# Kernel tuning notes

Hardware: AMD Instinct MI355X
Metric: run time of the kernel (lower is better)

Reference implementation:

```python
import jax, jax.numpy as jnp
import numpy as np

B, C, OC, H, W = 2, 64, 128, 96, 96
HD, DI, N, R, K = C // 2, C, 16, 2, 4  # VSSBlock: hidden=C/2, d_inner=2*hidden=C, d_state, dt_rank, 4 scan dirs
EPS = 1e-5


def _conv(x, w, b, pad, groups=1):
    y = jax.lax.conv_general_dilated(x, w, (1, 1), pad, feature_group_count=groups,
                                     dimension_numbers=('NCHW', 'OIHW', 'NCHW'))
    return y + b[None, :, None, None]


def _ln(x, w, b):
    m = x.mean(-1, keepdims=True)
    v = x.var(-1, keepdims=True)
    return (x - m) * jax.lax.rsqrt(v + EPS) * w + b


def _selective_scan(xs, dts, Bs, Cs, A, D):
    # xs, dts: (B,K,DI,L); Bs, Cs: (B,K,N,L); A: (K,DI,N); D: (K,DI)
    dts = jax.nn.softplus(dts)

    def step(h, inp):
        u_t, dt_t, B_t, C_t = inp
        dA = jnp.exp(dt_t[..., None] * A)                         # (B,K,DI,N)
        h = dA * h + (dt_t * u_t)[..., None] * B_t[:, :, None, :]
        return h, jnp.einsum('bkdn,bkn->bkd', h, C_t)

    seq = (jnp.moveaxis(xs, -1, 0), jnp.moveaxis(dts, -1, 0),
           jnp.moveaxis(Bs, -1, 0), jnp.moveaxis(Cs, -1, 0))
    h0 = jnp.zeros(xs.shape[:3] + (A.shape[-1],), xs.dtype)
    _, ys = jax.lax.scan(step, h0, seq)
    return jnp.moveaxis(ys, 0, -1) + D[None, :, :, None] * xs


def _vss_block(x, ln_w, ln_b, in_w, conv_w, conv_b, xproj_w, dtproj_w, dtproj_b,
               A_logs, Ds, on_w, on_b, out_w):
    # x: (B,H,W,HD); VMamba SS2D with 4-direction cross-scan + residual
    b, hh, ww, _ = x.shape
    L = hh * ww
    h = _ln(x, ln_w, ln_b)
    xz = h @ in_w                                   # (B,H,W,2*DI)
    xp, z = jnp.split(xz, 2, axis=-1)
    xc = jnp.transpose(xp, (0, 3, 1, 2))            # (B,DI,H,W)
    xc = jax.nn.silu(_conv(xc, conv_w, conv_b, ((1, 1), (1, 1)), groups=DI))
    x_flat = xc.reshape(b, DI, L)
    x_wh = jnp.transpose(xc, (0, 1, 3, 2)).reshape(b, DI, L)
    x2 = jnp.stack([x_flat, x_wh], axis=1)
    xs = jnp.concatenate([x2, jnp.flip(x2, -1)], axis=1)      # (B,4,DI,L)
    x_dbl = jnp.einsum('bkdl,kcd->bkcl', xs, xproj_w)
    dts, Bs, Cs = jnp.split(x_dbl, [R, R + N], axis=2)
    dts = jnp.einsum('bkrl,kdr->bkdl', dts, dtproj_w) + dtproj_b[None, :, :, None]
    A = -jnp.exp(A_logs)
    ys = _selective_scan(xs, dts, Bs, Cs, A, Ds)              # (B,4,DI,L)
    inv = jnp.flip(ys[:, 2:4], -1)
    unwh = lambda t: jnp.transpose(t.reshape(b, DI, ww, hh), (0, 1, 3, 2)).reshape(b, DI, L)
    y = ys[:, 0] + inv[:, 0] + unwh(ys[:, 1]) + unwh(inv[:, 1])
    y = jnp.transpose(y.reshape(b, DI, hh, ww), (0, 2, 3, 1))
    y = _ln(y, on_w, on_b) * jax.nn.silu(z)
    return x + y @ out_w


def _forward(x, ms_dw33_w, ms_dw33_b, ms_in_w, ms_in_b, ms_scale,
             vss_ln_w, vss_ln_b, vss_in_w, vss_conv_w, vss_conv_b, vss_xproj_w,
             vss_dtproj_w, vss_dtproj_b, vss_A_logs, vss_Ds, vss_on_w, vss_on_b, vss_out_w,
             ma_conv_w, ma_conv_b, adw_h_w, adw_h_b, adw_w_w, adw_w_b,
             pw_w, pw_b, bn_w, bn_b, bn_mean, bn_var):
    vss = (vss_ln_w, vss_ln_b, vss_in_w, vss_conv_w, vss_conv_b, vss_xproj_w,
           vss_dtproj_w, vss_dtproj_b, vss_A_logs, vss_Ds, vss_on_w, vss_on_b, vss_out_w)
    # --- MambaSplit (shared VSSBlock applied to both channel halves) ---
    xd = _conv(x, ms_dw33_w, ms_dw33_b, ((1, 1), (1, 1)), groups=C)
    x1, x2 = jnp.split(xd, 2, axis=1)

    def branch(xp):
        y = _vss_block(jnp.transpose(xp, (0, 2, 3, 1)), *vss)
        return ms_scale * xp + jnp.transpose(y, (0, 3, 1, 2))

    xm = jnp.concatenate([branch(x1), branch(x2)], axis=1)
    m = xm.mean((2, 3), keepdims=True)
    v = xm.var((2, 3), keepdims=True)
    xm = (xm - m) * jax.lax.rsqrt(v + EPS) * ms_in_w[None, :, None, None] + ms_in_b[None, :, None, None]
    xm = jax.nn.leaky_relu(xm, 0.01)
    # --- MaxAvg (global avg+max pool -> 3x3 conv on 1x1 map -> sigmoid gate) ---
    pooled = jnp.concatenate([x.mean((2, 3), keepdims=True), x.max((2, 3), keepdims=True)], axis=1)
    gate = jax.nn.sigmoid(_conv(pooled, ma_conv_w, ma_conv_b, ((1, 1), (1, 1))))
    xs_ = xm + gate * x
    # --- AxialDW ---
    xs_ = xs_ + _conv(xs_, adw_h_w, adw_h_b, ((1, 1), (0, 0)), groups=C) \
              + _conv(xs_, adw_w_w, adw_w_b, ((0, 0), (1, 1)), groups=C)
    # --- BN (eval) + ReLU, 1x1 conv, 2x2 maxpool ---
    skip = jax.nn.relu((xs_ - bn_mean[None, :, None, None]) * jax.lax.rsqrt(bn_var[None, :, None, None] + EPS)
                       * bn_w[None, :, None, None] + bn_b[None, :, None, None])
    out = _conv(skip, pw_w, pw_b, ((0, 0), (0, 0)))
    down = jax.lax.reduce_window(out, -jnp.inf, jax.lax.max, (1, 1, 2, 2), (1, 1, 2, 2), 'VALID')
    return down, skip


def setup_inputs() -> dict:
    key = jax.random.key(0)
    ks = jax.random.split(key, 16)
    r = lambda i, shape, s=0.02: jax.random.normal(ks[i], shape, jnp.float32) * s
    return {
        'x': jax.random.normal(ks[0], (B, C, H, W), jnp.float32),
        'ms_dw33_w': r(1, (C, 1, 3, 3), 0.1), 'ms_dw33_b': jnp.zeros(C),
        'ms_in_w': jnp.ones(C), 'ms_in_b': jnp.zeros(C),
        'ms_scale': jnp.ones((1,)),
        'vss_ln_w': jnp.ones(HD), 'vss_ln_b': jnp.zeros(HD),
        'vss_in_w': r(2, (HD, 2 * DI)),
        'vss_conv_w': r(3, (DI, 1, 3, 3), 0.1), 'vss_conv_b': jnp.zeros(DI),
        'vss_xproj_w': r(4, (K, R + 2 * N, DI)),
        'vss_dtproj_w': r(5, (K, DI, R), 0.1), 'vss_dtproj_b': r(6, (K, DI), 0.1),
        'vss_A_logs': jnp.tile(jnp.log(jnp.arange(1, N + 1, dtype=jnp.float32)), (K, DI, 1)),
        'vss_Ds': jnp.ones((K, DI)),
        'vss_on_w': jnp.ones(DI), 'vss_on_b': jnp.zeros(DI),
        'vss_out_w': r(7, (DI, HD)),
        'ma_conv_w': r(8, (C, 2 * C, 3, 3), 0.05), 'ma_conv_b': jnp.zeros(C),
        'adw_h_w': r(9, (C, 1, 3, 1), 0.1), 'adw_h_b': jnp.zeros(C),
        'adw_w_w': r(10, (C, 1, 1, 3), 0.1), 'adw_w_b': jnp.zeros(C),
        'pw_w': r(11, (OC, C, 1, 1)), 'pw_b': jnp.zeros(OC),
        'bn_w': jnp.ones(C), 'bn_b': jnp.zeros(C),
        'bn_mean': jnp.zeros(C), 'bn_var': jnp.ones(C),
    }


def reference(x, ms_dw33_w, ms_dw33_b, ms_in_w, ms_in_b, ms_scale,
              vss_ln_w, vss_ln_b, vss_in_w, vss_conv_w, vss_conv_b, vss_xproj_w,
              vss_dtproj_w, vss_dtproj_b, vss_A_logs, vss_Ds, vss_on_w, vss_on_b, vss_out_w,
              ma_conv_w, ma_conv_b, adw_h_w, adw_h_b, adw_w_w, adw_w_b,
              pw_w, pw_b, bn_w, bn_b, bn_mean, bn_var):
    return _forward(x, ms_dw33_w, ms_dw33_b, ms_in_w, ms_in_b, ms_scale,
                    vss_ln_w, vss_ln_b, vss_in_w, vss_conv_w, vss_conv_b, vss_xproj_w,
                    vss_dtproj_w, vss_dtproj_b, vss_A_logs, vss_Ds, vss_on_w, vss_on_b, vss_out_w,
                    ma_conv_w, ma_conv_b, adw_h_w, adw_h_b, adw_w_w, adw_w_b,
                    pw_w, pw_b, bn_w, bn_b, bn_mean, bn_var)
```

## Files before the change

kernel.cpp:

```cpp
#include <hip/hip_runtime.h>
#include <hip/hip_bf16.h>

typedef __hip_bfloat16 bf16;
#define DEV __device__ __forceinline__

constexpr int B_ = 2, C_ = 64, H_ = 96, W_ = 96, L_ = 9216;
constexpr int HD_ = 32, DI_ = 64, N_ = 16, K_ = 4, BB_ = 4;
constexpr int OC_ = 128;
constexpr int CH_ = 384, CL_ = 24;
constexpr int SEGN = 32, SEGC = 12;
constexpr int BROW = 20;
constexpr float EPSF = 1e-5f;
constexpr int DOWN_SZ = B_ * OC_ * 48 * 48;

typedef __attribute__((ext_vector_type(8))) short short8;
typedef __attribute__((ext_vector_type(4))) float f32x4;
typedef __attribute__((ext_vector_type(2))) float f32x2;

DEV float softplusf(float x) { return x > 15.f ? x : __logf(1.f + __expf(x)); }
DEV float b2f(bf16 v) { return __bfloat162float(v); }
DEV float lo16f(unsigned v) { return __uint_as_float(v << 16); }
DEV float hi16f(unsigned v) { return __uint_as_float(v & 0xffff0000u); }
DEV f32x2 pk2(unsigned w) { f32x2 r = {lo16f(w), hi16f(w)}; return r; }
DEV f32x2 lo2(f32x4 q) { f32x2 r = {q.x, q.y}; return r; }
DEV f32x2 hi2(f32x4 q) { f32x2 r = {q.z, q.w}; return r; }
DEV unsigned pkbf(float a, float b) {
  __hip_bfloat162 t;
  t.x = __float2bfloat16(a);
  t.y = __float2bfloat16(b);
  return *reinterpret_cast<unsigned*>(&t);
}
DEV void unpk8(uint4 a, float* v) {
  v[0] = lo16f(a.x); v[1] = hi16f(a.x); v[2] = lo16f(a.y); v[3] = hi16f(a.y);
  v[4] = lo16f(a.z); v[5] = hi16f(a.z); v[6] = lo16f(a.w); v[7] = hi16f(a.w);
}
DEV void unpk(uint4 a, uint4 b, float* v) {
  unpk8(a, v); unpk8(b, v + 8);
}

__constant__ float kLogN[16] = {
  0.0f, 0.69314718f, 1.09861229f, 1.38629436f, 1.60943791f, 1.79175947f,
  1.94591015f, 2.07944154f, 2.19722458f, 2.30258509f, 2.39789527f,
  2.48490665f, 2.56494936f, 2.63905733f, 2.70805020f, 2.77258872f};

DEV void pow_tree2(float e1, f32x2* ep) {
  float e2 = e1 * e1;
  ep[0].x = e1; ep[0].y = e2;
  f32x2 b2v = {e2, e2};
  ep[1] = ep[0] * b2v;
  float e4 = ep[1].y;
  f32x2 b4v = {e4, e4};
  ep[2] = ep[0] * b4v;
  ep[3] = ep[1] * b4v;
  float e8 = ep[3].y;
  f32x2 b8v = {e8, e8};
  ep[4] = ep[0] * b8v;
  ep[5] = ep[1] * b8v;
  ep[6] = ep[2] * b8v;
  ep[7] = ep[3] * b8v;
}

__global__ __launch_bounds__(256, 4) void k_front(
    const float* __restrict__ x, const float* __restrict__ dw33w,
    const float* __restrict__ dw33b, const float* __restrict__ lnw,
    const float* __restrict__ lnb, const float* __restrict__ inw,
    const float* __restrict__ xpw, const float* __restrict__ alog,
    float* __restrict__ xd, bf16* __restrict__ xzAh, bf16* __restrict__ xzBh,
    bf16* __restrict__ wh, float* __restrict__ aux) {
  int bb = blockIdx.y, t = threadIdx.x;
  int b = bb & 1, co = (bb >> 1) * HD_;
  int idx0 = blockIdx.x * 32;
  if (bb == 0) {
    int i = blockIdx.x * 256 + t;
    if (i < 144 * 64) {
      int n = i >> 6;
      wh[i] = __float2bfloat16(n < 136 ? xpw[i] : 0.f);
    }
    if (blockIdx.x == 0) {
      int kd = t;
      const float* al = alog + kd * N_;
      float a0 = al[0];
      bool lin = true;
#pragma unroll
      for (int n = 1; n < N_; n++) lin = lin && (fabsf(al[n] - a0 - kLogN[n]) < 3e-5f);
      aux[kd] = -__expf(a0);
      aux[256 + kd] = lin ? 1.f : 0.f;
#pragma unroll
      for (int n = 0; n < N_; n++) aux[512 + kd * N_ + n] = -__expf(al[n]);
    }
  }
  __shared__ float xds[32 * 36];
  __shared__ float meanA[32], rstdA[32];
  for (int i = t; i < 1024; i += 256) {
    int cl = i >> 5, ii = i & 31;
    int sp = idx0 + ii, wi = sp % 96, hi = sp / 96;
    int cg = b * C_ + co + cl;
    float acc = dw33b[co + cl];
#pragma unroll
    for (int dy = -1; dy <= 1; dy++) {
      int hh = hi + dy; if (hh < 0 || hh >= H_) continue;
#pragma unroll
      for (int dx = -1; dx <= 1; dx++) {
        int ww = wi + dx; if (ww < 0 || ww >= W_) continue;
        acc = fmaf(x[(size_t)cg * L_ + sp + dy * 96 + dx],
                   dw33w[(co + cl) * 9 + (dy + 1) * 3 + (dx + 1)], acc);
      }
    }
    xds[cl * 36 + ii] = acc;
    xd[(size_t)cg * L_ + sp] = acc;
  }
  __syncthreads();
  if (t < 32) {
    float s = 0.f, sq = 0.f;
#pragma unroll
    for (int c = 0; c < 32; c++) { float v = xds[c * 36 + t]; s += v; sq = fmaf(v, v, sq); }
    float mean = s * (1.f / HD_);
    float var = sq * (1.f / HD_) - mean * mean;
    meanA[t] = mean; rstdA[t] = rsqrtf(var + EPSF);
  }
  __syncthreads();
  for (int i = t; i < 1024; i += 256) {
    int c = i >> 5, idx = i & 31;
    float v = xds[c * 36 + idx];
    xds[c * 36 + idx] = (v - meanA[idx]) * rstdA[idx] * lnw[c] + lnb[c];
  }
  __syncthreads();
  int oc = t & 127, g = t >> 7;
  float acc[16];
#pragma unroll
  for (int j = 0; j < 16; j++) acc[j] = 0.f;
  for (int c = 0; c < 32; c++) {
    float wv = inw[c * 128 + oc];
    const float4* row = reinterpret_cast<const float4*>(&xds[c * 36 + g * 16]);
#pragma unroll
    for (int j4 = 0; j4 < 4; j4++) {
      float4 xv = row[j4];
      acc[j4 * 4 + 0] = fmaf(xv.x, wv, acc[j4 * 4 + 0]);
      acc[j4 * 4 + 1] = fmaf(xv.y, wv, acc[j4 * 4 + 1]);
      acc[j4 * 4 + 2] = fmaf(xv.z, wv, acc[j4 * 4 + 2]);
      acc[j4 * 4 + 3] = fmaf(xv.w, wv, acc[j4 * 4 + 3]);
    }
  }
  int occ = oc & 63;
  if (oc < 64) {
#pragma unroll
    for (int j = 0; j < 16; j++)
      xzAh[(size_t)(bb * L_ + idx0 + g * 16 + j) * 64 + occ] = __float2bfloat16(acc[j]);
  } else {
#pragma unroll
    for (int j = 0; j < 16; j++)
      xzBh[(size_t)(bb * L_ + idx0 + g * 16 + j) * 64 + occ] = __float2bfloat16(acc[j]);
  }
}

__global__ void k_dwsilu(const bf16* __restrict__ xzAh, const float* __restrict__ cw,
                         const float* __restrict__ cb, bf16* __restrict__ xch,
                         bf16* __restrict__ xcht) {
  int t = blockIdx.x * 256 + threadIdx.x;
  int d = t & 63, idx = (t >> 6) % L_, bb = t / (L_ * DI_);
  int wi = idx % W_, hi = idx / W_;
  float acc = cb[d];
#pragma unroll
  for (int dy = -1; dy <= 1; dy++) {
    int hh = hi + dy; if (hh < 0 || hh >= H_) continue;
#pragma unroll
    for (int dx = -1; dx <= 1; dx++) {
      int ww = wi + dx; if (ww < 0 || ww >= W_) continue;
      acc = fmaf(b2f(xzAh[(size_t)(bb * L_ + hh * W_ + ww) * 64 + d]),
                 cw[d * 9 + (dy + 1) * 3 + (dx + 1)], acc);
    }
  }
  acc = acc / (1.f + __expf(-acc));
  bf16 v = __float2bfloat16(acc);
  xch[t] = v;
  int idx_t = wi * 96 + hi;
  xcht[((size_t)bb * L_ + idx_t) * DI_ + d] = v;
}

__global__ __launch_bounds__(256, 4) void k_xdbl_mfma(
    const bf16* __restrict__ xch, const bf16* __restrict__ wh,
    float* __restrict__ xdblB, float* __restrict__ xdblC) {
  int w = threadIdx.x >> 6, lane = threadIdx.x & 63;
  int bb = blockIdx.y;
  int mtile = blockIdx.x * 4 + w;
  int idx0 = mtile * 16;
  int m = lane & 15, quad = lane >> 4;
  const bf16* arow = xch + ((size_t)bb * L_ + idx0 + m) * 64 + quad * 8;
  short8 a0 = *reinterpret_cast<const short8*>(arow);
  short8 a1 = *reinterpret_cast<const short8*>(arow + 32);
  int ntb = blockIdx.z * 3;
#pragma unroll
  for (int it = 0; it < 3; it++) {
    int nt = ntb + it;
    int n = nt * 16 + m;
    const bf16* brow = wh + n * 64 + quad * 8;
    short8 b0 = *reinterpret_cast<const short8*>(brow);
    short8 b1 = *reinterpret_cast<const short8*>(brow + 32);
    f32x4 acc = {0.f, 0.f, 0.f, 0.f};
    acc = __builtin_amdgcn_mfma_f32_16x16x32_bf16(a0, b0, acc, 0, 0, 0);
    acc = __builtin_amdgcn_mfma_f32_16x16x32_bf16(a1, b1, acc, 0, 0, 0);
    if (n < 136) {
      int k4 = (n >= 102) ? 3 : (n >= 68) ? 2 : (n >= 34) ? 1 : 0;
      int c = n - k4 * 34;
#pragma unroll
      for (int i = 0; i < 4; i++) {
        int r = idx0 + quad * 4 + i;
        int hi2 = r / 96, wi2 = r - hi2 * 96;
        int tr = wi2 * 96 + hi2;
        int ls = (k4 == 0) ? r : (k4 == 1) ? tr : (k4 == 2) ? (L_ - 1 - r) : (L_ - 1 - tr);
        size_t row = (size_t)(bb * K_ + k4) * L_ + ls;
        if (c < 2)       xdblB[row * BROW + 16 + c] = acc[i];
        else if (c < 18) xdblB[row * BROW + (c - 2)] = acc[i];
        else             xdblC[row * 16 + (c - 18)] = acc[i];
      }
    }
  }
}

__global__ __launch_bounds__(256, 4) void k_scan1(
    const float* __restrict__ xdblB, const bf16* __restrict__ xch,
    const bf16* __restrict__ xcht, const float* __restrict__ dtw,
    const float* __restrict__ dtb, const float* __restrict__ aux,
    bf16* __restrict__ hbuf, float* __restrict__ ssum) {
  int w = threadIdx.x >> 6, d = threadIdx.x & 63;
  int bx = blockIdx.x;
  int chunk = bx * 4 + w, k = blockIdx.y, bb = blockIdx.z;
  const float* bB = xdblB + (size_t)(bb * K_ + k) * L_ * BROW;
  __shared__ __align__(16) float sB[96 * BROW];
  {
    const uint4* src = (const uint4*)(bB + (size_t)bx * 96 * BROW);
    uint4* dst = (uint4*)sB;
    for (int i = threadIdx.x; i < 480; i += 256) dst[i] = src[i];
  }
  __syncthreads();
  float w0 = dtw[(k * DI_ + d) * 2 + 0], w1 = dtw[(k * DI_ + d) * 2 + 1];
  float bia = dtb[k * DI_ + d];
  float A1 = aux[k * 64 + d];
  bool chain = (__ballot(aux[256 + k * 64 + d] > 0.5f) == ~0ull);
  const bf16* ub = ((k & 1) ? xcht : xch) + (size_t)bb * L_ * DI_;
  int ls0 = chunk * CL_;
  int uidx0 = (k & 2) ? (L_ - 1 - ls0) : ls0;
  int ustep = (k & 2) ? -1 : 1;
  float S = 0.f;
  size_t base = (size_t)((bb * K_ + k) * CH_ + chunk) * DI_ + d;
  if (chain) {
    float uv[CL_];
    const bf16* up = ub + (size_t)uidx0 * DI_ + d;
#pragma unroll
    for (int s = 0; s < CL_; s++) uv[s] = b2f(up[s * ustep * DI_]);
    f32x2 h2[8];
#pragma unroll
    for (int i = 0; i < 8; i++) { h2[i].x = 0.f; h2[i].y = 0.f; }
#pragma unroll
    for (int s = 0; s < CL_; s++) {
      const float* p = sB + (w * CL_ + s) * BROW;
      f32x4 q0 = *(const f32x4*)p;
      f32x4 q1 = *(const f32x4*)(p + 4);
      f32x4 q2 = *(const f32x4*)(p + 8);
      f32x4 q3 = *(const f32x4*)(p + 12);
      f32x2 tt = *(const f32x2*)(p + 16);
      float dt = softplusf(fmaf(tt.x, w0, fmaf(tt.y, w1, bia)));
      S += dt;
      float du = dt * uv[s];
      f32x2 du2 = {du, du};
      f32x2 ep2[8];
      pow_tree2(__expf(dt * A1), ep2);
      h2[0] = ep2[0] * h2[0] + du2 * lo2(q0);
      h2[1] = ep2[1] * h2[1] + du2 * hi2(q0);
      h2[2] = ep2[2] * h2[2] + du2 * lo2(q1);
      h2[3] = ep2[3] * h2[3] + du2 * hi2(q1);
      h2[4] = ep2[4] * h2[4] + du2 * lo2(q2);
      h2[5] = ep2[5] * h2[5] + du2 * hi2(q2);
      h2[6] = ep2[6] * h2[6] + du2 * lo2(q3);
      h2[7] = ep2[7] * h2[7] + du2 * hi2(q3);
    }
    uint4 o0, o1;
    o0.x = pkbf(h2[0].x, h2[0].y); o0.y = pkbf(h2[1].x, h2[1].y);
    o0.z = pkbf(h2[2].x, h2[2].y); o0.w = pkbf(h2[3].x, h2[3].y);
    o1.x = pkbf(h2[4].x, h2[4].y); o1.y = pkbf(h2[5].x, h2[5].y);
    o1.z = pkbf(h2[6].x, h2[6].y); o1.w = pkbf(h2[7].x, h2[7].y);
    *(uint4*)(hbuf + base * N_) = o0;
    *(uint4*)(hbuf + base * N_ + 8) = o1;
  } else {
    float h[N_];
#pragma unroll
    for (int n = 0; n < N_; n++) h[n] = 0.f;
    float A[N_];
#pragma unroll
    for (int n = 0; n < N_; n++) A[n] = aux[512 + (k * 64 + d) * N_ + n];
    for (int s = 0; s < CL_; s++) {
      const float* p = sB + (w * CL_ + s) * BROW;
      float u = b2f(ub[(size_t)(uidx0 + s * ustep) * DI_ + d]);
      float dt = softplusf(fmaf(p[16], w0, fmaf(p[17], w1, bia)));
      S += dt;
      float du = dt * u;
#pragma unroll
      for (int n = 0; n < N_; n++) h[n] = fmaf(__expf(dt * A[n]), h[n], du * p[n]);
    }
#pragma unroll
    for (int n = 0; n < N_; n++) hbuf[base * N_ + n] = __float2bfloat16(h[n]);
  }
  ssum[base] = S;
}

__global__ __launch_bounds__(256, 4) void k_scan2(
    const float* __restrict__ aux, const float* __restrict__ ssum,
    bf16* __restrict__ hbuf, float* __restrict__ cumS,
    float* __restrict__ segH) {
  int tid = threadIdx.x;
  int r = tid & 7, seg = tid >> 3;
  int bi = blockIdx.x;
  int oct = bi & 1, d = (bi >> 1) & 63, kk = (bi >> 7) & 3, bb = bi >> 9;
  int n = oct * 8 + r;
  float A = aux[512 + (kk * 64 + d) * N_ + n];
  size_t row = (size_t)(bb * K_ + kk) * CH_ * DI_ + d;
  float hp = 0.f, Sc = 0.f;
#pragma unroll 4
  for (int j = 0; j < SEGC; j++) {
    int c = seg * SEGC + j;
    size_t sb = row + (size_t)c * DI_;
    float S = ssum[sb];
    float hl = b2f(hbuf[sb * N_ + n]);
    hbuf[sb * N_ + n] = __float2bfloat16(hp);
    if (n == 0) cumS[sb] = Sc;
    hp = fmaf(__expf(A * S), hp, hl);
    Sc += S;
  }
  __shared__ float sH[SEGN][8], sE[SEGN][8];
  sH[seg][r] = hp;
  sE[seg][r] = __expf(A * Sc);
  __syncthreads();
  if (tid < 8) {
    float h = 0.f;
    for (int s2 = 0; s2 < SEGN; s2++) {
      float Hs = sH[s2][tid];
      sH[s2][tid] = h;
      h = fmaf(sE[s2][tid], h, Hs);
    }
  }
  __syncthreads();
  size_t sbase = (size_t)(bb * K_ + kk) * SEGN + seg;
  segH[(sbase * DI_ + d) * N_ + n] = sH[seg][r];
}

__global__ __launch_bounds__(256, 4) void k_scan3(
    const float* __restrict__ xdblB, const float* __restrict__ xdblC,
    const bf16* __restrict__ xch, const bf16* __restrict__ xcht,
    const float* __restrict__ dtw, const float* __restrict__ dtb,
    const float* __restrict__ Dsw, const float* __restrict__ aux,
    const bf16* __restrict__ hbuf, const float* __restrict__ cumS,
    const float* __restrict__ segH, bf16* __restrict__ ydir) {
  int w = threadIdx.x >> 6, d = threadIdx.x & 63;
  int bx = blockIdx.x;
  int chunk = bx * 4 + w, k = blockIdx.y, bb = blockIdx.z;
  const float* bB = xdblB + (size_t)(bb * K_ + k) * L_ * BROW;
  const float* bC = xdblC + (size_t)(bb * K_ + k) * L_ * 16;
  __shared__ __align__(16) float sB[96 * BROW];
  __shared__ __align__(16) float sC[96 * 16];
  {
    const uint4* srcB = (const uint4*)(bB + (size_t)bx * 96 * BROW);
    uint4* dstB = (uint4*)sB;
    for (int i = threadIdx.x; i < 480; i += 256) dstB[i] = srcB[i];
    const uint4* srcC = (const uint4*)(bC + (size_t)bx * 96 * 16);
    uint4* dstC = (uint4*)sC;
    for (int i = threadIdx.x; i < 384; i += 256) dstC[i] = srcC[i];
  }
  __syncthreads();
  float w0 = dtw[(k * DI_ + d) * 2 + 0], w1 = dtw[(k * DI_ + d) * 2 + 1];
  float bia = dtb[k * DI_ + d];
  float Dk = Dsw[k * DI_ + d];
  float A1 = aux[k * 64 + d];
  bool chain = (__ballot(aux[256 + k * 64 + d] > 0.5f) == ~0ull);
  size_t base = (size_t)((bb * K_ + k) * CH_ + chunk) * DI_ + d;
  int seg = chunk / SEGC;
  size_t sbase = (size_t)(bb * K_ + k) * SEGN + seg;
  float Sc = cumS[base];
  const bf16* ub = ((k & 1) ? xcht : xch) + (size_t)bb * L_ * DI_;
  bf16* yb = ydir + (size_t)(bb * K_ + k) * L_ * DI_;
  int ls0 = chunk * CL_;
  int uidx0 = (k & 2) ? (L_ - 1 - ls0) : ls0;
  int ustep = (k & 2) ? -1 : 1;
  const bf16* hb = hbuf + base * N_;
  const float* Hin = segH + (sbase * DI_ + d) * N_;
  if (chain) {
    float uv[CL_];
    const bf16* up = ub + (size_t)uidx0 * DI_ + d;
#pragma unroll
    for (int s = 0; s < CL_; s++) uv[s] = b2f(up[s * ustep * DI_]);
    f32x2 h2[8];
    {
      uint4 qh0 = *(const uint4*)hb, qh1 = *(const uint4*)(hb + 8);
      h2[0] = pk2(qh0.x); h2[1] = pk2(qh0.y); h2[2] = pk2(qh0.z); h2[3] = pk2(qh0.w);
      h2[4] = pk2(qh1.x); h2[5] = pk2(qh1.y); h2[6] = pk2(qh1.z); h2[7] = pk2(qh1.w);
      f32x2 ep2[8];
      pow_tree2(__expf(A1 * Sc), ep2);
#pragma unroll
      for (int i = 0; i < 8; i++)
        h2[i] = ep2[i] * (*(const f32x2*)(Hin + 2 * i)) + h2[i];
    }
#pragma unroll
    for (int s = 0; s < CL_; s++) {
      int lr = w * CL_ + s;
      const float* p = sB + lr * BROW;
      const float* pc = sC + lr * 16;
      f32x4 q0 = *(const f32x4*)p;
      f32x4 q1 = *(const f32x4*)(p + 4);
      f32x4 q2 = *(const f32x4*)(p + 8);
      f32x4 q3 = *(const f32x4*)(p + 12);
      f32x2 tt = *(const f32x2*)(p + 16);
      f32x4 c0 = *(const f32x4*)pc;
      f32x4 c1 = *(const f32x4*)(pc + 4);
      f32x4 c2 = *(const f32x4*)(pc + 8);
      f32x4 c3 = *(const f32x4*)(pc + 12);
      float dt = softplusf(fmaf(tt.x, w0, fmaf(tt.y, w1, bia)));
      float du = dt * uv[s];
      f32x2 du2 = {du, du};
      f32x2 ep2[8];
      pow_tree2(__expf(dt * A1), ep2);
      f32x2 y2 = {0.f, 0.f};
      h2[0] = ep2[0] * h2[0] + du2 * lo2(q0);  y2 = h2[0] * lo2(c0) + y2;
      h2[1] = ep2[1] * h2[1] + du2 * hi2(q0);  y2 = h2[1] * hi2(c0) + y2;
      h2[2] = ep2[2] * h2[2] + du2 * lo2(q1);  y2 = h2[2] * lo2(c1) + y2;
      h2[3] = ep2[3] * h2[3] + du2 * hi2(q1);  y2 = h2[3] * hi2(c1) + y2;
      h2[4] = ep2[4] * h2[4] + du2 * lo2(q2);  y2 = h2[4] * lo2(c2) + y2;
      h2[5] = ep2[5] * h2[5] + du2 * hi2(q2);  y2 = h2[5] * hi2(c2) + y2;
      h2[6] = ep2[6] * h2[6] + du2 * lo2(q3);  y2 = h2[6] * lo2(c3) + y2;
      h2[7] = ep2[7] * h2[7] + du2 * hi2(q3);  y2 = h2[7] * hi2(c3) + y2;
      float y = fmaf(Dk, uv[s], y2.x + y2.y);
      yb[(size_t)(ls0 + s) * DI_ + d] = __float2bfloat16(y);
    }
  } else {
    float h[N_];
    {
      uint4 qh0 = *(const uint4*)hb, qh1 = *(const uint4*)(hb + 8);
      unpk(qh0, qh1, h);
#pragma unroll
      for (int n = 0; n < N_; n++) {
        float A = aux[512 + (k * 64 + d) * N_ + n];
        h[n] = fmaf(__expf(A * Sc), Hin[n], h[n]);
      }
    }
    float A[N_];
#pragma unroll
    for (int n = 0; n < N_; n++) A[n] = aux[512 + (k * 64 + d) * N_ + n];
    for (int s = 0; s < CL_; s++) {
      int lr = w * CL_ + s;
      const float* p = sB + lr * BROW;
      const float* pc = sC + lr * 16;
      float u = b2f(ub[(size_t)(uidx0 + s * ustep) * DI_ + d]);
      float dt = softplusf(fmaf(p[16], w0, fmaf(p[17], w1, bia)));
      float du = dt * u;
      float y = 0.f;
#pragma unroll
      for (int n = 0; n < N_; n++) {
        h[n] = fmaf(__expf(dt * A[n]), h[n], du * p[n]);
        y = fmaf(h[n], pc[n], y);
      }
      y = fmaf(Dk, u, y);
      yb[(size_t)(ls0 + s) * DI_ + d] = __float2bfloat16(y);
    }
  }
}

__global__ void k_combine(const bf16* __restrict__ ydir, const bf16* __restrict__ xzBh,
                          const float* __restrict__ xd, const float* __restrict__ onw,
                          const float* __restrict__ onb, const float* __restrict__ outw,
                          const float* __restrict__ mssc, float* __restrict__ xm) {
  int w = threadIdx.x >> 6, d = threadIdx.x & 63;
  int idx = blockIdx.x * 4 + w, bb = blockIdx.y;
  int b = bb & 1, co = (bb >> 1) * HD_;
  int hii = idx / 96, wii = idx - hii * 96;
  int lt = wii * 96 + hii;
  const bf16* yd = ydir + (size_t)bb * K_ * L_ * DI_;
  float y = b2f(yd[((size_t)0 * L_ + idx) * DI_ + d])
          + b2f(yd[((size_t)1 * L_ + lt) * DI_ + d])
          + b2f(yd[((size_t)2 * L_ + (L_ - 1 - idx)) * DI_ + d])
          + b2f(yd[((size_t)3 * L_ + (L_ - 1 - lt)) * DI_ + d]);
  float s = y, sq = y * y;
#pragma unroll
  for (int m = 1; m < 64; m <<= 1) { s += __shfl_xor(s, m, 64); sq += __shfl_xor(sq, m, 64); }
  float mean = s * (1.f / DI_);
  float var = sq * (1.f / DI_) - mean * mean;
  float rstd = rsqrtf(var + EPSF);
  float yn = (y - mean) * rstd * onw[d] + onb[d];
  float z = b2f(xzBh[(size_t)(bb * L_ + idx) * 64 + d]);
  float g = yn * (z / (1.f + __expf(-z)));
  __shared__ float gs[4][DI_];
  gs[w][d] = g;
  __syncthreads();
  if (d < HD_) {
    float acc = 0.f;
#pragma unroll
    for (int dd = 0; dd < DI_; dd++) acc = fmaf(gs[w][dd], outw[dd * HD_ + d], acc);
    size_t xi = (size_t)(b * C_ + co + d) * L_ + idx;
    float xp = xd[xi];
    xm[xi] = mssc[0] * xp + xp + acc;
  }
}

__global__ __launch_bounds__(1024) void k_stats(
    const float* __restrict__ xm, const float* __restrict__ x,
    float* __restrict__ inm, float* __restrict__ inr,
    float* __restrict__ xmean, float* __restrict__ xmax) {
  int bc = blockIdx.x, t = threadIdx.x;
  const float* pm = xm + (size_t)bc * L_;
  const float* px = x + (size_t)bc * L_;
  float s = 0.f, sq = 0.f, xs = 0.f, mx = -1e30f;
  for (int i = t; i < L_; i += 1024) {
    float v = pm[i]; s += v; sq = fmaf(v, v, sq);
    float xv = px[i]; xs += xv; mx = fmaxf(mx, xv);
  }
  __shared__ float red[64];
#pragma unroll
  for (int m = 1; m < 64; m <<= 1) {
    s += __shfl_xor(s, m, 64); sq += __shfl_xor(sq, m, 64);
    xs += __shfl_xor(xs, m, 64); mx = fmaxf(mx, __shfl_xor(mx, m, 64));
  }
  int wid = t >> 6;
  if ((t & 63) == 0) { red[wid] = s; red[16 + wid] = sq; red[32 + wid] = xs; red[48 + wid] = mx; }
  __syncthreads();
  if (t == 0) {
    s = 0.f; sq = 0.f; xs = 0.f; mx = -1e30f;
#pragma unroll
    for (int i = 0; i < 16; i++) {
      s += red[i]; sq += red[16 + i]; xs += red[32 + i]; mx = fmaxf(mx, red[48 + i]);
    }
    float mean = s * (1.f / L_);
    float var = sq * (1.f / L_) - mean * mean;
    inm[bc] = mean;
    inr[bc] = rsqrtf(var + EPSF);
    xmean[bc] = xs * (1.f / L_);
    xmax[bc] = mx;
  }
}

__global__ void k_axbn(const float* __restrict__ xm, const float* __restrict__ x,
                       const float* __restrict__ inm, const float* __restrict__ inr,
                       const float* __restrict__ msw, const float* __restrict__ msb,
                       const float* __restrict__ xmean, const float* __restrict__ xmax,
                       const float* __restrict__ maw, const float* __restrict__ mab,
                       const float* __restrict__ hw, const float* __restrict__ hb,
                       const float* __restrict__ wwt, const float* __restrict__ wb,
                       const float* __restrict__ bnw, const float* __restrict__ bnb,
                       const float* __restrict__ bnm, const float* __restrict__ bnv,
                       float* __restrict__ skipo) {
  constexpr int NEL = B_ * C_ * L_;
  int t0 = blockIdx.x * 256;
  int t = t0 + threadIdx.x;
  int bc = t0 / L_, c = bc & 63, b = bc >> 6;
  __shared__ float gsh;
  __shared__ float sxs[448];
  if (threadIdx.x < 64) {
    int ic = threadIdx.x;
    float p = xmean[b * 64 + ic] * maw[(c * 128 + ic) * 9 + 4]
            + xmax[b * 64 + ic] * maw[(c * 128 + 64 + ic) * 9 + 4];
#pragma unroll
    for (int m = 1; m < 64; m <<= 1) p += __shfl_xor(p, m, 64);
    if (ic == 0) gsh = 1.f / (1.f + __expf(-(p + mab[c])));
  }
  __syncthreads();
  float gate = gsh, im = inm[bc], ir = inr[bc], mw = msw[c], mb = msb[c];
  for (int i = threadIdx.x; i < 448; i += 256) {
    int tt = t0 - 96 + i;
    tt = tt < 0 ? 0 : (tt >= NEL ? NEL - 1 : tt);
    float v = xm[tt];
    v = (v - im) * ir * mw + mb;
    v = v > 0.f ? v : 0.01f * v;
    sxs[i] = v + gate * x[tt];
  }
  __syncthreads();
  int li = 96 + threadIdx.x;
  int wi = t % W_, hi = (t / W_) % H_;
  float a = sxs[li];
  float hacc = hb[c];
#pragma unroll
  for (int dy = -1; dy <= 1; dy++) {
    int hh = hi + dy; if (hh < 0 || hh >= H_) continue;
    hacc = fmaf(sxs[li + dy * 96], hw[c * 3 + dy + 1], hacc);
  }
  float wacc = wb[c];
#pragma unroll
  for (int dx = -1; dx <= 1; dx++) {
    int ww = wi + dx; if (ww < 0 || ww >= W_) continue;
    wacc = fmaf(sxs[li + dx], wwt[c * 3 + dx + 1], wacc);
  }
  float v = a + hacc + wacc;
  float sv = (v - bnm[c]) * rsqrtf(bnv[c] + EPSF) * bnw[c] + bnb[c];
  skipo[t] = fmaxf(sv, 0.f);
}

__global__ void k_pwpool(const float* __restrict__ skipo, const float* __restrict__ pww,
                         const float* __restrict__ pwb, float* __restrict__ down) {
  int h2 = blockIdx.x, b = blockIdx.y, t = threadIdx.x;
  int oc0 = blockIdx.z * 32;
  __shared__ __align__(8) float sk[64 * 192];
  for (int i = t; i < 64 * 192; i += 256) {
    int c = i / 192, rw = i % 192, r = rw / 96, wcol = rw % 96;
    sk[i] = skipo[((size_t)(b * C_ + c) * H_ + (2 * h2 + r)) * W_ + wcol];
  }
  __syncthreads();
  for (int o = t; o < 32 * 48; o += 256) {
    int oc = oc0 + o / 48, w2 = o % 48;
    float s0 = 0.f, s1 = 0.f, s2 = 0.f, s3 = 0.f;
#pragma unroll 8
    for (int c = 0; c < 64; c++) {
      float wv = pww[oc * 64 + c];
      const float2* sp = (const float2*)&sk[c * 192 + 2 * w2];
      float2 r0 = sp[0];
      float2 r1 = sp[48];
      s0 = fmaf(r0.x, wv, s0);
      s1 = fmaf(r0.y, wv, s1);
      s2 = fmaf(r1.x, wv, s2);
      s3 = fmaf(r1.y, wv, s3);
    }
    float v = fmaxf(fmaxf(s0, s1), fmaxf(s2, s3)) + pwb[oc];
    down[((size_t)(b * OC_ + oc) * 48 + h2) * 48 + w2] = v;
  }
}

extern "C" void kernel_launch(void* const* d_in, const int* in_sizes, int n_in,
                              void* d_out, int out_size, void* d_ws, size_t ws_size,
                              hipStream_t stream) {
  const float* x     = (const float*)d_in[0];
  const float* dw33w = (const float*)d_in[1];
  const float* dw33b = (const float*)d_in[2];
  const float* msw   = (const float*)d_in[3];
  const float* msb   = (const float*)d_in[4];
  const float* mssc  = (const float*)d_in[5];
  const float* lnw   = (const float*)d_in[6];
  const float* lnb   = (const float*)d_in[7];
  const float* inw   = (const float*)d_in[8];
  const float* cw    = (const float*)d_in[9];
  const float* cb    = (const float*)d_in[10];
  const float* xpw   = (const float*)d_in[11];
  const float* dtw   = (const float*)d_in[12];
  const float* dtb   = (const float*)d_in[13];
  const float* alog  = (const float*)d_in[14];
  const float* Dsw   = (const float*)d_in[15];
  const float* onw   = (const float*)d_in[16];
  const float* onb   = (const float*)d_in[17];
  const float* outw  = (const float*)d_in[18];
  const float* maw   = (const float*)d_in[19];
  const float* mab   = (const float*)d_in[20];
  const float* ahw   = (const float*)d_in[21];
  const float* ahb   = (const float*)d_in[22];
  const float* aww   = (const float*)d_in[23];
  const float* awb   = (const float*)d_in[24];
  const float* pww   = (const float*)d_in[25];
  const float* pwb   = (const float*)d_in[26];
  const float* bnw   = (const float*)d_in[27];
  const float* bnb   = (const float*)d_in[28];
  const float* bnm   = (const float*)d_in[29];
  const float* bnv   = (const float*)d_in[30];

  float* ws = (float*)d_ws;
  float* xd    = ws;
  float* hreg  = xd + 1179648;
  bf16*  hbuf  = (bf16*)hreg;
  bf16*  xzAh  = (bf16*)hreg;
  bf16*  xzBh  = (bf16*)(hreg + 1179648);
  float* xdblB = hreg + 1179648 + 1179648;
  float* xdblC = xdblB + 2949120;
  float* ssum  = xdblC + 2359296;
  bf16*  ydir  = (bf16*)(ssum + 393216);
  float* xmR   = ssum + 393216 + 4718592;
  bf16*  xch   = (bf16*)xmR;
  float* xm    = xmR;
  float* st    = xmR + 1179648;
  float* inm = st, *inr = st + 128, *xmean = st + 256, *xmaxv = st + 384;
  float* aux   = st + 512;
  bf16*  wh    = (bf16*)(aux + 4608);
  float* cumS  = aux + 4608 + 4608;
  float* segH  = cumS + 393216;
  bf16*  xcht  = (bf16*)(segH + 524288 + 32768);

  float* outp = (float*)d_out;
  float* down = outp;
  float* skipo = outp + DOWN_SZ;

  dim3 b256(256);
  int nEl = B_ * C_ * L_;

  k_front<<<dim3(L_ / 32, BB_), b256, 0, stream>>>(x, dw33w, dw33b, lnw, lnb, inw,
                                                   xpw, alog, xd, xzAh, xzBh, wh, aux);
  k_dwsilu<<<dim3(BB_ * L_ * DI_ / 256), b256, 0, stream>>>(xzAh, cw, cb, xch, xcht);
  k_xdbl_mfma<<<dim3(L_ / 64, BB_, 3), b256, 0, stream>>>(xch, wh, xdblB, xdblC);
  k_scan1<<<dim3(CH_ / 4, K_, BB_), b256, 0, stream>>>(xdblB, xch, xcht, dtw, dtb, aux, hbuf, ssum);
  k_scan2<<<dim3(BB_ * K_ * DI_ * 2), b256, 0, stream>>>(aux, ssum, hbuf, cumS, segH);
  k_scan3<<<dim3(CH_ / 4, K_, BB_), b256, 0, stream>>>(xdblB, xdblC, xch, xcht, dtw, dtb, Dsw,
                                                      aux, hbuf, cumS, segH, ydir);
  k_combine<<<dim3(L_ / 4, BB_), b256, 0, stream>>>(ydir, xzBh, xd, onw, onb, outw, mssc, xm);
  k_stats<<<dim3(B_ * C_), dim3(1024), 0, stream>>>(xm, x, inm, inr, xmean, xmaxv);
  k_axbn<<<dim3((nEl + 255) / 256), b256, 0, stream>>>(xm, x, inm, inr, msw, msb, xmean, xmaxv,
                                                      maw, mab, ahw, ahb, aww, awb,
                                                      bnw, bnb, bnm, bnv, skipo);
  k_pwpool<<<dim3(48, B_, 4), b256, 0, stream>>>(skipo, pww, pwb, down);
}
```

Measured before the change: 321.6 us.

## Vectorize dwsilu/stats, split scan2 into two kernels, parallelize combine projection

The depthwise conv+SiLU kernel now handles two channels per thread with packed 32-bit bf16 loads and stores. The middle scan stage is split into a per-segment kernel and a separate cross-segment prefix kernel, with a new segS buffer replacing the in-block shared-memory serial prefix. This spreads the work across many more threads and gives better memory coalescing. The combine kernel uses all 64 lanes for the output projection, with float4 shared reads and a shuffle reduction. The stats kernel reads float4. Together these target memory-access width and idle lanes, at the cost of an extra kernel launch and more global traffic for the segment prefix.

```diff
diff --git a/kernel.cpp b/kernel.cpp
--- a/kernel.cpp
+++ b/kernel.cpp
@@ -157,24 +157,30 @@
                          const float* __restrict__ cb, bf16* __restrict__ xch,
                          bf16* __restrict__ xcht) {
   int t = blockIdx.x * 256 + threadIdx.x;
-  int d = t & 63, idx = (t >> 6) % L_, bb = t / (L_ * DI_);
+  int dp = t & 31, idx = (t >> 5) % L_, bb = t / (L_ * 32);
+  int d0 = dp * 2;
   int wi = idx % W_, hi = idx / W_;
-  float acc = cb[d];
+  const unsigned* src = (const unsigned*)xzAh;
+  float acc0 = cb[d0], acc1 = cb[d0 + 1];
 #pragma unroll
   for (int dy = -1; dy <= 1; dy++) {
     int hh = hi + dy; if (hh < 0 || hh >= H_) continue;
 #pragma unroll
     for (int dx = -1; dx <= 1; dx++) {
       int ww = wi + dx; if (ww < 0 || ww >= W_) continue;
-      acc = fmaf(b2f(xzAh[(size_t)(bb * L_ + hh * W_ + ww) * 64 + d]),
-                 cw[d * 9 + (dy + 1) * 3 + (dx + 1)], acc);
-    }
-  }
-  acc = acc / (1.f + __expf(-acc));
-  bf16 v = __float2bfloat16(acc);
-  xch[t] = v;
+      unsigned v = src[(size_t)(bb * L_ + hh * W_ + ww) * 32 + dp];
+      float w0 = cw[d0 * 9 + (dy + 1) * 3 + (dx + 1)];
+      float w1 = cw[(d0 + 1) * 9 + (dy + 1) * 3 + (dx + 1)];
+      acc0 = fmaf(lo16f(v), w0, acc0);
+      acc1 = fmaf(hi16f(v), w1, acc1);
+    }
+  }
+  acc0 = acc0 / (1.f + __expf(-acc0));
+  acc1 = acc1 / (1.f + __expf(-acc1));
+  unsigned out = pkbf(acc0, acc1);
+  ((unsigned*)xch)[t] = out;
   int idx_t = wi * 96 + hi;
-  xcht[((size_t)bb * L_ + idx_t) * DI_ + d] = v;
+  ((unsigned*)xcht)[((size_t)bb * L_ + idx_t) * 32 + dp] = out;
 }
 
 __global__ __launch_bounds__(256, 4) void k_xdbl_mfma(
@@ -303,15 +309,12 @@
   ssum[base] = S;
 }
 
-__global__ __launch_bounds__(256, 4) void k_scan2(
+__global__ __launch_bounds__(256, 4) void k_scan2a(
     const float* __restrict__ aux, const float* __restrict__ ssum,
     bf16* __restrict__ hbuf, float* __restrict__ cumS,
-    float* __restrict__ segH) {
-  int tid = threadIdx.x;
-  int r = tid & 7, seg = tid >> 3;
-  int bi = blockIdx.x;
-  int oct = bi & 1, d = (bi >> 1) & 63, kk = (bi >> 7) & 3, bb = bi >> 9;
-  int n = oct * 8 + r;
+    float* __restrict__ segH, float* __restrict__ segS) {
+  int t = blockIdx.x * 256 + threadIdx.x;
+  int n = t & 15, d = (t >> 4) & 63, kk = (t >> 10) & 3, bb = (t >> 12) & 3, seg = t >> 14;
   float A = aux[512 + (kk * 64 + d) * N_ + n];
   size_t row = (size_t)(bb * K_ + kk) * CH_ * DI_ + d;
   float hp = 0.f, Sc = 0.f;
@@ -326,21 +329,25 @@
     hp = fmaf(__expf(A * S), hp, hl);
     Sc += S;
   }
-  __shared__ float sH[SEGN][8], sE[SEGN][8];
-  sH[seg][r] = hp;
-  sE[seg][r] = __expf(A * Sc);
-  __syncthreads();
-  if (tid < 8) {
-    float h = 0.f;
-    for (int s2 = 0; s2 < SEGN; s2++) {
-      float Hs = sH[s2][tid];
-      sH[s2][tid] = h;
-      h = fmaf(sE[s2][tid], h, Hs);
-    }
-  }
-  __syncthreads();
   size_t sbase = (size_t)(bb * K_ + kk) * SEGN + seg;
-  segH[(sbase * DI_ + d) * N_ + n] = sH[seg][r];
+  segH[(sbase * DI_ + d) * N_ + n] = hp;
+  if (n == 0) segS[sbase * DI_ + d] = Sc;
+}
+
+__global__ void k_scan2b(const float* __restrict__ aux, float* __restrict__ segH,
+                         const float* __restrict__ segS) {
+  int t = blockIdx.x * 256 + threadIdx.x;
+  int n = t & 15, d = (t >> 4) & 63, kk = (t >> 10) & 3, bb = t >> 12;
+  float A = aux[512 + (kk * 64 + d) * N_ + n];
+  float hp = 0.f;
+  for (int seg = 0; seg < SEGN; seg++) {
+    size_t sbase = (size_t)(bb * K_ + kk) * SEGN + seg;
+    size_t si = (sbase * DI_ + d) * N_ + n;
+    float H = segH[si];
+    float E = __expf(A * segS[sbase * DI_ + d]);
+    segH[si] = hp;
+    hp = fmaf(E, hp, H);
+  }
 }
 
 __global__ __launch_bounds__(256, 4) void k_scan3(
@@ -485,13 +492,24 @@
   float yn = (y - mean) * rstd * onw[d] + onb[d];
   float z = b2f(xzBh[(size_t)(bb * L_ + idx) * 64 + d]);
   float g = yn * (z / (1.f + __expf(-z)));
-  __shared__ float gs[4][DI_];
+  __shared__ __align__(16) float gs[4][DI_];
   gs[w][d] = g;
   __syncthreads();
+  int dh = d & 31;
+  int ddb = (d >= 32) ? 32 : 0;
+  const float* grow = &gs[w][ddb];
+  float acc = 0.f;
+#pragma unroll
+  for (int j = 0; j < 8; j++) {
+    float4 gv = *(const float4*)(grow + j * 4);
+    int dd = ddb + j * 4;
+    acc = fmaf(gv.x, outw[(dd + 0) * HD_ + dh], acc);
+    acc = fmaf(gv.y, outw[(dd + 1) * HD_ + dh], acc);
+    acc = fmaf(gv.z, outw[(dd + 2) * HD_ + dh], acc);
+    acc = fmaf(gv.w, outw[(dd + 3) * HD_ + dh], acc);
+  }
+  acc += __shfl_xor(acc, 32, 64);
   if (d < HD_) {
-    float acc = 0.f;
-#pragma unroll
-    for (int dd = 0; dd < DI_; dd++) acc = fmaf(gs[w][dd], outw[dd * HD_ + d], acc);
     size_t xi = (size_t)(b * C_ + co + d) * L_ + idx;
     float xp = xd[xi];
     xm[xi] = mssc[0] * xp + xp + acc;
@@ -503,12 +521,17 @@
     float* __restrict__ inm, float* __restrict__ inr,
     float* __restrict__ xmean, float* __restrict__ xmax) {
   int bc = blockIdx.x, t = threadIdx.x;
-  const float* pm = xm + (size_t)bc * L_;
-  const float* px = x + (size_t)bc * L_;
+  const float4* pm4 = (const float4*)(xm + (size_t)bc * L_);
+  const float4* px4 = (const float4*)(x + (size_t)bc * L_);
   float s = 0.f, sq = 0.f, xs = 0.f, mx = -1e30f;
-  for (int i = t; i < L_; i += 1024) {
-    float v = pm[i]; s += v; sq = fmaf(v, v, sq);
-    float xv = px[i]; xs += xv; mx = fmaxf(mx, xv);
+  for (int i = t; i < L_ / 4; i += 1024) {
+    float4 v = pm4[i];
+    s += (v.x + v.y) + (v.z + v.w);
+    sq = fmaf(v.x, v.x, sq); sq = fmaf(v.y, v.y, sq);
+    sq = fmaf(v.z, v.z, sq); sq = fmaf(v.w, v.w, sq);
+    float4 xv = px4[i];
+    xs += (xv.x + xv.y) + (xv.z + xv.w);
+    mx = fmaxf(mx, fmaxf(fmaxf(xv.x, xv.y), fmaxf(xv.z, xv.w)));
   }
   __shared__ float red[64];
 #pragma unroll
@@ -672,7 +695,8 @@
   bf16*  wh    = (bf16*)(aux + 4608);
   float* cumS  = aux + 4608 + 4608;
   float* segH  = cumS + 393216;
-  bf16*  xcht  = (bf16*)(segH + 524288 + 32768);
+  float* segS  = segH + 524288;
+  bf16*  xcht  = (bf16*)(segS + 32768);
 
   float* outp = (float*)d_out;
   float* down = outp;
@@ -683,10 +707,11 @@
 
   k_front<<<dim3(L_ / 32, BB_), b256, 0, stream>>>(x, dw33w, dw33b, lnw, lnb, inw,
                                                    xpw, alog, xd, xzAh, xzBh, wh, aux);
-  k_dwsilu<<<dim3(BB_ * L_ * DI_ / 256), b256, 0, stream>>>(xzAh, cw, cb, xch, xcht);
+  k_dwsilu<<<dim3(BB_ * L_ * 32 / 256), b256, 0, stream>>>(xzAh, cw, cb, xch, xcht);
   k_xdbl_mfma<<<dim3(L_ / 64, BB_, 3), b256, 0, stream>>>(xch, wh, xdblB, xdblC);
   k_scan1<<<dim3(CH_ / 4, K_, BB_), b256, 0, stream>>>(xdblB, xch, xcht, dtw, dtb, aux, hbuf, ssum);
-  k_scan2<<<dim3(BB_ * K_ * DI_ * 2), b256, 0, stream>>>(aux, ssum, hbuf, cumS, segH);
+  k_scan2a<<<dim3(BB_ * K_ * SEGN * DI_ * N_ / 256), b256, 0, stream>>>(aux, ssum, hbuf, cumS, segH, segS);
+  k_scan2b<<<dim3(BB_ * K_ * DI_ * N_ / 256), b256, 0, stream>>>(aux, segH, segS);
   k_scan3<<<dim3(CH_ / 4, K_, BB_), b256, 0, stream>>>(xdblB, xdblC, xch, xcht, dtw, dtb, Dsw,
                                                       aux, hbuf, cumS, segH, ydir);
   k_combine<<<dim3(L_ / 4, BB_), b256, 0, stream>>>(ydir, xzBh, xd, onw, onb, outw, mssc, xm);
```

After: 286.1 us. -11.0%, faster.
